# Kernel tuning notes

Measured on AMD Instinct MI355X. Metric: run time of the kernel, lower is better.

The kernel has to match this reference:

```python
import jax, jax.numpy as jnp
import numpy as np
from jax import lax

B, S, D, H, TMAX = 8, 512, 256, 4, 20
DH = D // H
LAMBDA = 1e-3
V_TH = 1.0


def setup_inputs() -> dict:
    key = jax.random.key(0)
    ks = jax.random.split(key, 10)
    sc = lambda n: 1.0 / np.sqrt(n)
    f32 = jnp.float32
    return {
        "x": jax.random.normal(ks[0], (B, S, D), f32),
        "Wq": (jax.random.normal(ks[1], (D, D), f32) * sc(D)),
        "Wk": (jax.random.normal(ks[2], (D, D), f32) * sc(D)),
        "Wv": (jax.random.normal(ks[3], (D, D), f32) * sc(D)),
        "Wo": (jax.random.normal(ks[4], (D, D), f32) * sc(D)),
        "bo": jnp.zeros((D,), f32),
        "Wg1": (jax.random.normal(ks[5], (D, 32), f32) * sc(D)),
        "bg1": jnp.zeros((32,), f32),
        "Wg2": (jax.random.normal(ks[6], (32, 1), f32) * sc(32)),
        "bg2": jnp.zeros((1,), f32),
        "alpha_q": jnp.asarray(np.exp(-1 / 5.0), f32),
        "beta_q": jnp.asarray(np.exp(-1 / 20.0), f32),
        "alpha_k": jnp.asarray(np.exp(-1 / 5.0), f32),
        "beta_k": jnp.asarray(np.exp(-1 / 20.0), f32),
        "alpha_v": jnp.asarray(np.exp(-1 / 5.0), f32),
        "beta_v": jnp.asarray(np.exp(-1 / 20.0), f32),
    }


def _lif_spikes(x, alpha, beta, Ti):
    """LIF recurrence with CONSTANT input x per step, sequential only over T.
    x: [B,S,D], Ti: [B,S] int. Returns spikes [B,S,TMAX,D], zeroed for t >= Ti
    (equivalent to the original per-(b,s) loop that only runs Ti steps,
    since the recurrence is causal)."""
    zeros = jnp.zeros_like(x)
    tmask = jnp.arange(TMAX)

    def step(carry, t):
        v, i = carry
        i = alpha * i + x
        v = beta * v + i
        spk = (v >= V_TH).astype(x.dtype)
        v = v * (1.0 - spk)  # v_reset = 0
        spk_out = spk * (t < Ti).astype(x.dtype)[..., None]
        return (v, i), spk_out

    _, spks = lax.scan(step, (zeros, zeros), tmask)
    return jnp.moveaxis(spks, 0, 2)  # [B,S,T,D]


def reference(x, Wq, Wk, Wv, Wo, bo, Wg1, bg1, Wg2, bg2,
              alpha_q, beta_q, alpha_k, beta_k, alpha_v, beta_v):
    q = x @ Wq
    k = x @ Wk
    v = x @ Wv
    # adaptive window gate -> Ti in [1, TMAX]
    gate = jax.nn.sigmoid(jax.nn.relu(x @ Wg1 + bg1) @ Wg2 + bg2)[..., 0]  # [B,S]
    Ti = jnp.clip(jnp.ceil(gate * TMAX), 1, TMAX).astype(jnp.int32)
    q_spk = _lif_spikes(q, alpha_q, beta_q, Ti)  # [B,S,T,D]
    k_spk = _lif_spikes(k, alpha_k, beta_k, Ti)
    v_spk = _lif_spikes(v, alpha_v, beta_v, Ti)
    qh = q_spk.reshape(B, S, TMAX, H, DH)
    kh = k_spk.reshape(B, S, TMAX, H, DH)
    vh = v_spk.reshape(B, S, TMAX, H, DH)
    scale = DH ** -0.5
    Sraw = jnp.einsum('bithd,bjthd->bhij', qh, kh) * scale  # [B,H,S,S]
    W = jax.nn.softmax(Sraw, axis=-1)
    v_mean = vh.mean(axis=2)  # [B,S,H,DH] (mean over full T, zeros beyond Ti)
    out = jnp.einsum('bhij,bjhd->bihd', W, v_mean).reshape(B, S, D)
    out = out @ Wo + bo
    reg = LAMBDA * Ti.astype(jnp.float32).mean()
    return out, reg, Ti, W
```

## Files before the change

### kernel.cpp

```cpp
#include <hip/hip_runtime.h>
#include <hip/hip_bf16.h>

typedef unsigned long long u64;
typedef unsigned short u16;
typedef __attribute__((ext_vector_type(8))) short short8;
typedef __attribute__((ext_vector_type(4))) float float4_t;

#define BB 8
#define SS 512
#define DD 256
#define HH 4
#define TT 20
#define BS (BB*SS)

#define REG_OFF (BS*DD)
#define TI_OFF  (REG_OFF+1)
#define W_OFF   (TI_OFF+BS)

static __device__ __forceinline__ u16 f2bf(float f) {
    __hip_bfloat16 h = __float2bfloat16(f);
    return *reinterpret_cast<u16*>(&h);
}

__global__ __launch_bounds__(256) void k_proj_lif(
    const float* __restrict__ x, const float* __restrict__ Wq,
    const float* __restrict__ Wk, const float* __restrict__ Wv,
    const float* __restrict__ Wg1, const float* __restrict__ bg1,
    const float* __restrict__ Wg2, const float* __restrict__ bg2,
    const float* __restrict__ aq, const float* __restrict__ bq_,
    const float* __restrict__ ak, const float* __restrict__ bk_,
    const float* __restrict__ av, const float* __restrict__ bv_,
    u64* __restrict__ qpack, u64* __restrict__ kpack,
    u16* __restrict__ vmb, float* __restrict__ ti_out)
{
    __shared__ float xl[8][DD];
    __shared__ int til[8];
    const int tid  = threadIdx.x;
    const int proj = blockIdx.y;
    const int tok0 = blockIdx.x * 8;

    #pragma unroll
    for (int m = 0; m < 8; ++m) xl[m][tid] = x[(size_t)(tok0+m)*DD + tid];
    __syncthreads();

    {
        int tok = tid >> 5, c = tid & 31;
        float acc = bg1[c];
        for (int r = 0; r < DD; ++r) acc += xl[tok][r] * Wg1[r*32 + c];
        float hrelu = acc > 0.f ? acc : 0.f;
        float term  = hrelu * Wg2[c];
        #pragma unroll
        for (int msk = 16; msk >= 1; msk >>= 1) term += __shfl_xor(term, msk, 64);
        if (c == 0) {
            float g  = term + bg2[0];
            float sg = 1.f / (1.f + expf(-g));
            int ti = (int)ceilf(sg * (float)TT);
            ti = ti < 1 ? 1 : (ti > TT ? TT : ti);
            til[tok] = ti;
            if (proj == 0) ti_out[tok0 + tok] = (float)ti;
        }
    }
    __syncthreads();

    const float* W    = proj == 0 ? Wq  : (proj == 1 ? Wk  : Wv);
    const float alpha = proj == 0 ? *aq : (proj == 1 ? *ak : *av);
    const float beta  = proj == 0 ? *bq_: (proj == 1 ? *bk_: *bv_);

    float acc[8] = {0,0,0,0,0,0,0,0};
    for (int r = 0; r < DD; ++r) {
        float w = W[r*DD + tid];
        #pragma unroll
        for (int i = 0; i < 8; ++i) acc[i] += xl[i][r] * w;
    }

    const int lane = tid & 63;
    const int h    = tid >> 6;
    u64* pack = (proj == 0) ? qpack : kpack;

    if (proj < 2) {
        for (int i = 0; i < 8; ++i) {
            int ti = til[i];
            float vv = 0.f, cur = 0.f;
            u64 myw = 0ull;
            #pragma unroll
            for (int t = 0; t < TT; ++t) {
                cur = alpha*cur + acc[i];
                vv  = beta*vv + cur;
                bool s = (vv >= 1.f);
                u64 bal = __ballot(s);
                if (s) vv = 0.f;
                if (lane == t && t < ti) myw = bal;
            }
            if (lane < TT) pack[((size_t)(tok0+i)*HH + h)*TT + lane] = myw;
        }
    } else {
        for (int i = 0; i < 8; ++i) {
            int ti = til[i];
            float vv = 0.f, cur = 0.f;
            float cnt = 0.f;
            #pragma unroll
            for (int t = 0; t < TT; ++t) {
                cur = alpha*cur + acc[i];
                vv  = beta*vv + cur;
                bool s = (vv >= 1.f);
                if (s) { vv = 0.f; if (t < ti) cnt += 1.f; }
            }
            vmb[(size_t)(tok0+i)*DD + tid] = f2bf(cnt * 0.05f);
        }
    }
}

__global__ __launch_bounds__(256) void k_reg(const float* __restrict__ ti, float* __restrict__ reg)
{
    __shared__ float ps[4];
    int tid = threadIdx.x;
    float s = 0.f;
    for (int m = 0; m < 16; ++m) s += ti[m*256 + tid];
    for (int msk = 32; msk >= 1; msk >>= 1) s += __shfl_xor(s, msk, 64);
    if ((tid & 63) == 0) ps[tid >> 6] = s;
    __syncthreads();
    if (tid == 0) reg[0] = 1e-3f * (ps[0]+ps[1]+ps[2]+ps[3]) / 4096.f;
}

__global__ __launch_bounds__(256) void k_attn(
    const u64* __restrict__ qpack, const u64* __restrict__ kpack,
    const u16* __restrict__ vmb,
    float* __restrict__ Wout, float* __restrict__ attn)
{
    __shared__ u64 ql[16][TT];
    __shared__ __align__(16) u16 CP[16*SS];
    const int tid  = threadIdx.x;
    const int tile = blockIdx.x & 31;
    const int h    = (blockIdx.x >> 5) & 3;
    const int b    = blockIdx.x >> 7;
    const int i0   = tile * 16;
    const int lane = tid & 63, wv = tid >> 6;

    for (int idx = tid; idx < 16*TT; idx += 256) {
        int i = idx / TT, t = idx - i*TT;
        ql[i][t] = qpack[((size_t)(b*SS + i0 + i)*HH + h)*TT + t];
    }

    u64 kr0[TT], kr1[TT];
    {
        const u64* kp0 = &kpack[((size_t)(b*SS + tid      )*HH + h)*TT];
        const u64* kp1 = &kpack[((size_t)(b*SS + tid + 256)*HH + h)*TT];
        #pragma unroll
        for (int t = 0; t < TT; ++t) { kr0[t] = kp0[t]; kr1[t] = kp1[t]; }
    }
    __syncthreads();

    for (int i = 0; i < 16; ++i) {
        int c0 = 0, c1 = 0;
        #pragma unroll
        for (int t = 0; t < TT; ++t) {
            u64 q = ql[i][t];
            c0 += __popcll(q & kr0[t]);
            c1 += __popcll(q & kr1[t]);
        }
        CP[i*SS + tid]       = (u16)c0;
        CP[i*SS + tid + 256] = (u16)c1;
    }
    __syncthreads();

    for (int rr = 0; rr < 4; ++rr) {
        const int i = wv*4 + rr;
        float sv[8];
        float m = -1e30f;
        #pragma unroll
        for (int k2 = 0; k2 < 8; ++k2) {
            sv[k2] = (float)CP[i*SS + lane + 64*k2] * 0.125f;
            m = fmaxf(m, sv[k2]);
        }
        #pragma unroll
        for (int msk = 32; msk >= 1; msk >>= 1) m = fmaxf(m, __shfl_xor(m, msk, 64));
        float sum = 0.f;
        #pragma unroll
        for (int k2 = 0; k2 < 8; ++k2) { sv[k2] = expf(sv[k2] - m); sum += sv[k2]; }
        #pragma unroll
        for (int msk = 32; msk >= 1; msk >>= 1) sum += __shfl_xor(sum, msk, 64);
        float inv = 1.f / sum;
        size_t wbase = ((size_t)((b*HH + h)*SS) + i0 + i) * SS;
        #pragma unroll
        for (int k2 = 0; k2 < 8; ++k2) {
            int j = lane + 64*k2;
            float wval = sv[k2] * inv;
            Wout[wbase + j] = wval;
            CP[(i*SS + j) ^ ((i & 7) << 3)] = f2bf(wval);
        }
    }
    __syncthreads();

    const int n0 = wv * 16;
    const int mr = lane & 15;
    const int g  = lane >> 4;
    float4_t acc = {0.f, 0.f, 0.f, 0.f};
    const u16* vb_base = vmb + (size_t)b*SS*DD + h*64 + n0 + mr;
    for (int ks = 0; ks < 16; ++ks) {
        int k = ks*32 + g*8;
        int aidx = (mr*SS + k) ^ ((mr & 7) << 3);
        short8 a = *reinterpret_cast<const short8*>(&CP[aidx]);
        union { u16 u[8]; short8 v; } bu;
        const u16* vb = vb_base + (size_t)k*DD;
        #pragma unroll
        for (int j = 0; j < 8; ++j) bu.u[j] = vb[(size_t)j*DD];
        acc = __builtin_amdgcn_mfma_f32_16x16x32_bf16(a, bu.v, acc, 0, 0, 0);
    }
    #pragma unroll
    for (int r = 0; r < 4; ++r) {
        int row = g*4 + r;
        attn[(size_t)(b*SS + i0 + row)*DD + h*64 + n0 + mr] = acc[r];
    }
}

__global__ __launch_bounds__(256) void k_outproj(
    const float* __restrict__ attn, const float* __restrict__ Wo,
    const float* __restrict__ bo, float* __restrict__ out)
{
    __shared__ float al[4][DD];
    const int tid  = threadIdx.x;
    const int tok0 = blockIdx.x * 4;
    #pragma unroll
    for (int m = 0; m < 4; ++m) al[m][tid] = attn[(size_t)(tok0+m)*DD + tid];
    __syncthreads();
    float acc[4] = {0,0,0,0};
    for (int r = 0; r < DD; ++r) {
        float w = Wo[r*DD + tid];
        #pragma unroll
        for (int i = 0; i < 4; ++i) acc[i] += al[i][r] * w;
    }
    float bb = bo[tid];
    #pragma unroll
    for (int i = 0; i < 4; ++i) out[(size_t)(tok0+i)*DD + tid] = acc[i] + bb;
}

extern "C" void kernel_launch(void* const* d_in, const int* in_sizes, int n_in,
                              void* d_out, int out_size, void* d_ws, size_t ws_size,
                              hipStream_t stream)
{
    (void)in_sizes; (void)n_in; (void)out_size; (void)ws_size;
    const float* x   = (const float*)d_in[0];
    const float* Wq  = (const float*)d_in[1];
    const float* Wk  = (const float*)d_in[2];
    const float* Wv  = (const float*)d_in[3];
    const float* Wo  = (const float*)d_in[4];
    const float* bo  = (const float*)d_in[5];
    const float* Wg1 = (const float*)d_in[6];
    const float* bg1 = (const float*)d_in[7];
    const float* Wg2 = (const float*)d_in[8];
    const float* bg2 = (const float*)d_in[9];
    const float* aq  = (const float*)d_in[10];
    const float* bq  = (const float*)d_in[11];
    const float* ak  = (const float*)d_in[12];
    const float* bk  = (const float*)d_in[13];
    const float* av  = (const float*)d_in[14];
    const float* bv  = (const float*)d_in[15];
    float* out = (float*)d_out;

    u64* qp = (u64*)d_ws;
    u64* kp = qp + (size_t)BS*HH*TT;
    u16* vmb = (u16*)(kp + (size_t)BS*HH*TT);
    float* attnbuf = (float*)(vmb + (size_t)BS*DD);

    dim3 gproj(512, 3);
    k_proj_lif<<<gproj, 256, 0, stream>>>(x, Wq, Wk, Wv, Wg1, bg1, Wg2, bg2,
        aq, bq, ak, bk, av, bv, qp, kp, vmb, out + TI_OFF);
    k_reg<<<1, 256, 0, stream>>>(out + TI_OFF, out + REG_OFF);
    k_attn<<<1024, 256, 0, stream>>>(qp, kp, vmb, out + W_OFF, attnbuf);
    k_outproj<<<1024, 256, 0, stream>>>(attnbuf, Wo, bo, out);
}
```

Measured before the change: 118.3 us.

## Split gate into separate kernel and transpose LDS tiles for vectorized projection loads

Moves the gate MLP out of the projection kernel into its own kernel, so it is computed once per token instead of once for each of the three projections; the projection kernel now reads Ti from global memory. The projection and output-projection kernels store the token tile transposed in shared memory, so each weight row pairs with two float4 LDS reads covering eight tokens. The output projection also processes eight tokens per block with half as many blocks, which doubles reuse of each Wo load. The cost is an extra kernel launch and a dependency between the gate and projection kernels.

```diff
diff --git a/kernel.cpp b/kernel.cpp
--- a/kernel.cpp
+++ b/kernel.cpp
@@ -22,44 +22,55 @@
     return *reinterpret_cast<u16*>(&h);
 }
 
+__global__ __launch_bounds__(256) void k_gate(
+    const float* __restrict__ x,
+    const float* __restrict__ Wg1, const float* __restrict__ bg1,
+    const float* __restrict__ Wg2, const float* __restrict__ bg2,
+    float* __restrict__ ti_out)
+{
+    __shared__ float xl[8][DD];
+    const int tid  = threadIdx.x;
+    const int tok0 = blockIdx.x * 8;
+    #pragma unroll
+    for (int m = 0; m < 8; ++m) xl[m][tid] = x[(size_t)(tok0+m)*DD + tid];
+    __syncthreads();
+
+    const int tok = tid >> 5, c = tid & 31;
+    float acc = bg1[c];
+    #pragma unroll 4
+    for (int r = 0; r < DD; ++r) acc += xl[tok][r] * Wg1[r*32 + c];
+    float hrelu = acc > 0.f ? acc : 0.f;
+    float term  = hrelu * Wg2[c];
+    #pragma unroll
+    for (int msk = 16; msk >= 1; msk >>= 1) term += __shfl_xor(term, msk, 64);
+    if (c == 0) {
+        float g  = term + bg2[0];
+        float sg = 1.f / (1.f + expf(-g));
+        int ti = (int)ceilf(sg * (float)TT);
+        ti = ti < 1 ? 1 : (ti > TT ? TT : ti);
+        ti_out[tok0 + tok] = (float)ti;
+    }
+}
+
 __global__ __launch_bounds__(256) void k_proj_lif(
     const float* __restrict__ x, const float* __restrict__ Wq,
     const float* __restrict__ Wk, const float* __restrict__ Wv,
-    const float* __restrict__ Wg1, const float* __restrict__ bg1,
-    const float* __restrict__ Wg2, const float* __restrict__ bg2,
     const float* __restrict__ aq, const float* __restrict__ bq_,
     const float* __restrict__ ak, const float* __restrict__ bk_,
     const float* __restrict__ av, const float* __restrict__ bv_,
+    const float* __restrict__ ti_in,
     u64* __restrict__ qpack, u64* __restrict__ kpack,
-    u16* __restrict__ vmb, float* __restrict__ ti_out)
-{
-    __shared__ float xl[8][DD];
+    u16* __restrict__ vmb)
+{
+    __shared__ float xl[DD][8];
     __shared__ int til[8];
     const int tid  = threadIdx.x;
     const int proj = blockIdx.y;
     const int tok0 = blockIdx.x * 8;
 
     #pragma unroll
-    for (int m = 0; m < 8; ++m) xl[m][tid] = x[(size_t)(tok0+m)*DD + tid];
-    __syncthreads();
-
-    {
-        int tok = tid >> 5, c = tid & 31;
-        float acc = bg1[c];
-        for (int r = 0; r < DD; ++r) acc += xl[tok][r] * Wg1[r*32 + c];
-        float hrelu = acc > 0.f ? acc : 0.f;
-        float term  = hrelu * Wg2[c];
-        #pragma unroll
-        for (int msk = 16; msk >= 1; msk >>= 1) term += __shfl_xor(term, msk, 64);
-        if (c == 0) {
-            float g  = term + bg2[0];
-            float sg = 1.f / (1.f + expf(-g));
-            int ti = (int)ceilf(sg * (float)TT);
-            ti = ti < 1 ? 1 : (ti > TT ? TT : ti);
-            til[tok] = ti;
-            if (proj == 0) ti_out[tok0 + tok] = (float)ti;
-        }
-    }
+    for (int m = 0; m < 8; ++m) xl[tid][m] = x[(size_t)(tok0+m)*DD + tid];
+    if (tid < 8) til[tid] = (int)ti_in[tok0 + tid];
     __syncthreads();
 
     const float* W    = proj == 0 ? Wq  : (proj == 1 ? Wk  : Wv);
@@ -67,10 +78,13 @@
     const float beta  = proj == 0 ? *bq_: (proj == 1 ? *bk_: *bv_);
 
     float acc[8] = {0,0,0,0,0,0,0,0};
+    #pragma unroll 4
     for (int r = 0; r < DD; ++r) {
         float w = W[r*DD + tid];
-        #pragma unroll
-        for (int i = 0; i < 8; ++i) acc[i] += xl[i][r] * w;
+        float4_t x0 = *reinterpret_cast<const float4_t*>(&xl[r][0]);
+        float4_t x1 = *reinterpret_cast<const float4_t*>(&xl[r][4]);
+        acc[0] += x0.x*w; acc[1] += x0.y*w; acc[2] += x0.z*w; acc[3] += x0.w*w;
+        acc[4] += x1.x*w; acc[5] += x1.y*w; acc[6] += x1.z*w; acc[7] += x1.w*w;
     }
 
     const int lane = tid & 63;
@@ -217,21 +231,24 @@
     const float* __restrict__ attn, const float* __restrict__ Wo,
     const float* __restrict__ bo, float* __restrict__ out)
 {
-    __shared__ float al[4][DD];
-    const int tid  = threadIdx.x;
-    const int tok0 = blockIdx.x * 4;
-    #pragma unroll
-    for (int m = 0; m < 4; ++m) al[m][tid] = attn[(size_t)(tok0+m)*DD + tid];
-    __syncthreads();
-    float acc[4] = {0,0,0,0};
+    __shared__ float al[DD][8];
+    const int tid  = threadIdx.x;
+    const int tok0 = blockIdx.x * 8;
+    #pragma unroll
+    for (int m = 0; m < 8; ++m) al[tid][m] = attn[(size_t)(tok0+m)*DD + tid];
+    __syncthreads();
+    float acc[8] = {0,0,0,0,0,0,0,0};
+    #pragma unroll 4
     for (int r = 0; r < DD; ++r) {
         float w = Wo[r*DD + tid];
-        #pragma unroll
-        for (int i = 0; i < 4; ++i) acc[i] += al[i][r] * w;
+        float4_t a0 = *reinterpret_cast<const float4_t*>(&al[r][0]);
+        float4_t a1 = *reinterpret_cast<const float4_t*>(&al[r][4]);
+        acc[0] += a0.x*w; acc[1] += a0.y*w; acc[2] += a0.z*w; acc[3] += a0.w*w;
+        acc[4] += a1.x*w; acc[5] += a1.y*w; acc[6] += a1.z*w; acc[7] += a1.w*w;
     }
     float bb = bo[tid];
     #pragma unroll
-    for (int i = 0; i < 4; ++i) out[(size_t)(tok0+i)*DD + tid] = acc[i] + bb;
+    for (int i = 0; i < 8; ++i) out[(size_t)(tok0+i)*DD + tid] = acc[i] + bb;
 }
 
 extern "C" void kernel_launch(void* const* d_in, const int* in_sizes, int n_in,
@@ -262,10 +279,11 @@
     u16* vmb = (u16*)(kp + (size_t)BS*HH*TT);
     float* attnbuf = (float*)(vmb + (size_t)BS*DD);
 
+    k_gate<<<512, 256, 0, stream>>>(x, Wg1, bg1, Wg2, bg2, out + TI_OFF);
+    k_reg<<<1, 256, 0, stream>>>(out + TI_OFF, out + REG_OFF);
     dim3 gproj(512, 3);
-    k_proj_lif<<<gproj, 256, 0, stream>>>(x, Wq, Wk, Wv, Wg1, bg1, Wg2, bg2,
-        aq, bq, ak, bk, av, bv, qp, kp, vmb, out + TI_OFF);
-    k_reg<<<1, 256, 0, stream>>>(out + TI_OFF, out + REG_OFF);
+    k_proj_lif<<<gproj, 256, 0, stream>>>(x, Wq, Wk, Wv,
+        aq, bq, ak, bk, av, bv, out + TI_OFF, qp, kp, vmb);
     k_attn<<<1024, 256, 0, stream>>>(qp, kp, vmb, out + W_OFF, attnbuf);
-    k_outproj<<<1024, 256, 0, stream>>>(attnbuf, Wo, bo, out);
-}
+    k_outproj<<<512, 256, 0, stream>>>(attnbuf, Wo, bo, out);
+}
```

After: 127.1 us. 7.5% more time.

## Split gate kernel, retile projections with float4 split-K, transpose V means for attention

Applied to the files above, without the earlier changes.

Moves the gate MLP into its own kernel so it is no longer recomputed by all three projection blocks. The Q/K/V and output projections now process 16 tokens per 512-thread block using float4 weight loads and a two-way split-K reduction through shared memory. V spike means are stored transposed so the attention MFMA B-fragment becomes one 16-byte load instead of eight strided loads. The reg reduction is folded into the output projection kernel. The cost is an extra launch plus added shared-memory traffic and barriers for the split-K reduction.

```diff
diff --git a/kernel.cpp b/kernel.cpp
--- a/kernel.cpp
+++ b/kernel.cpp
@@ -22,109 +22,159 @@
     return *reinterpret_cast<u16*>(&h);
 }
 
-__global__ __launch_bounds__(256) void k_proj_lif(
+__global__ __launch_bounds__(256) void k_gate(
+    const float* __restrict__ x,
+    const float* __restrict__ Wg1, const float* __restrict__ bg1,
+    const float* __restrict__ Wg2, const float* __restrict__ bg2,
+    float* __restrict__ ti_out)
+{
+    __shared__ float wgl[DD*32];
+    __shared__ float xl[16][DD];
+    const int tid  = threadIdx.x;
+    const int tok0 = blockIdx.x * 16;
+
+    #pragma unroll
+    for (int i = 0; i < 8; ++i) {
+        int j = i*256 + tid;
+        *reinterpret_cast<float4_t*>(&wgl[j*4]) =
+            *reinterpret_cast<const float4_t*>(&Wg1[j*4]);
+    }
+    #pragma unroll
+    for (int m = 0; m < 16; ++m) xl[m][tid] = x[(size_t)(tok0+m)*DD + tid];
+    __syncthreads();
+
+    const int tok = tid >> 4;
+    const int cq  = tid & 15;
+    const int c   = cq * 2;
+    float a0 = 0.f, a1 = 0.f;
+    #pragma unroll 8
+    for (int r = 0; r < DD; ++r) {
+        float xv = xl[tok][r];
+        a0 += xv * wgl[r*32 + c];
+        a1 += xv * wgl[r*32 + c + 1];
+    }
+    a0 += bg1[c]; a1 += bg1[c+1];
+    a0 = a0 > 0.f ? a0 : 0.f;
+    a1 = a1 > 0.f ? a1 : 0.f;
+    float term = a0 * Wg2[c] + a1 * Wg2[c+1];
+    #pragma unroll
+    for (int msk = 8; msk >= 1; msk >>= 1) term += __shfl_xor(term, msk, 64);
+    if (cq == 0) {
+        float g  = term + bg2[0];
+        float sg = 1.f / (1.f + expf(-g));
+        int ti = (int)ceilf(sg * (float)TT);
+        ti = ti < 1 ? 1 : (ti > TT ? TT : ti);
+        ti_out[tok0 + tok] = (float)ti;
+    }
+}
+
+__global__ __launch_bounds__(512) void k_proj_lif(
     const float* __restrict__ x, const float* __restrict__ Wq,
     const float* __restrict__ Wk, const float* __restrict__ Wv,
-    const float* __restrict__ Wg1, const float* __restrict__ bg1,
-    const float* __restrict__ Wg2, const float* __restrict__ bg2,
     const float* __restrict__ aq, const float* __restrict__ bq_,
     const float* __restrict__ ak, const float* __restrict__ bk_,
     const float* __restrict__ av, const float* __restrict__ bv_,
+    const float* __restrict__ ti_in,
     u64* __restrict__ qpack, u64* __restrict__ kpack,
-    u16* __restrict__ vmb, float* __restrict__ ti_out)
-{
-    __shared__ float xl[8][DD];
-    __shared__ int til[8];
+    u16* __restrict__ vmbT)
+{
+    __shared__ __align__(16) union {
+        float xt[DD][16];
+        float red[2][16][DD];
+    } sm;
+    __shared__ int til[16];
     const int tid  = threadIdx.x;
     const int proj = blockIdx.y;
-    const int tok0 = blockIdx.x * 8;
-
-    #pragma unroll
-    for (int m = 0; m < 8; ++m) xl[m][tid] = x[(size_t)(tok0+m)*DD + tid];
-    __syncthreads();
+    const int tok0 = blockIdx.x * 16;
 
     {
-        int tok = tid >> 5, c = tid & 31;
-        float acc = bg1[c];
-        for (int r = 0; r < DD; ++r) acc += xl[tok][r] * Wg1[r*32 + c];
-        float hrelu = acc > 0.f ? acc : 0.f;
-        float term  = hrelu * Wg2[c];
-        #pragma unroll
-        for (int msk = 16; msk >= 1; msk >>= 1) term += __shfl_xor(term, msk, 64);
-        if (c == 0) {
-            float g  = term + bg2[0];
-            float sg = 1.f / (1.f + expf(-g));
-            int ti = (int)ceilf(sg * (float)TT);
-            ti = ti < 1 ? 1 : (ti > TT ? TT : ti);
-            til[tok] = ti;
-            if (proj == 0) ti_out[tok0 + tok] = (float)ti;
-        }
-    }
+        const int r = tid & 255, mh = tid >> 8;
+        #pragma unroll
+        for (int i = 0; i < 8; ++i) {
+            int m = mh*8 + i;
+            sm.xt[r][m] = x[(size_t)(tok0+m)*DD + r];
+        }
+    }
+    if (tid < 16) til[tid] = (int)ti_in[tok0 + tid];
     __syncthreads();
 
     const float* W    = proj == 0 ? Wq  : (proj == 1 ? Wk  : Wv);
     const float alpha = proj == 0 ? *aq : (proj == 1 ? *ak : *av);
     const float beta  = proj == 0 ? *bq_: (proj == 1 ? *bk_: *bv_);
 
-    float acc[8] = {0,0,0,0,0,0,0,0};
-    for (int r = 0; r < DD; ++r) {
-        float w = W[r*DD + tid];
-        #pragma unroll
-        for (int i = 0; i < 8; ++i) acc[i] += xl[i][r] * w;
+    const int w  = tid >> 6, l = tid & 63;
+    const int kh = w >> 2;
+    const int tg = w & 3;
+
+    float4_t a[4];
+    #pragma unroll
+    for (int i = 0; i < 4; ++i) a[i] = (float4_t){0.f, 0.f, 0.f, 0.f};
+
+    const float* Wp = W + (size_t)(kh*128)*DD + l*4;
+    #pragma unroll 4
+    for (int r0 = 0; r0 < 128; ++r0) {
+        float4_t wf = *reinterpret_cast<const float4_t*>(Wp + (size_t)r0*DD);
+        float4_t xv = *reinterpret_cast<const float4_t*>(&sm.xt[kh*128 + r0][tg*4]);
+        a[0] += wf*xv.x; a[1] += wf*xv.y; a[2] += wf*xv.z; a[3] += wf*xv.w;
+    }
+    __syncthreads();
+    #pragma unroll
+    for (int i = 0; i < 4; ++i)
+        *reinterpret_cast<float4_t*>(&sm.red[kh][tg*4 + i][l*4]) = a[i];
+    __syncthreads();
+
+    const int col = tid & 255, th = tid >> 8;
+    float val[8];
+    #pragma unroll
+    for (int i = 0; i < 8; ++i) {
+        int m = th*8 + i;
+        val[i] = sm.red[0][m][col] + sm.red[1][m][col];
     }
 
     const int lane = tid & 63;
-    const int h    = tid >> 6;
-    u64* pack = (proj == 0) ? qpack : kpack;
-
+    const int h    = (tid >> 6) & 3;
     if (proj < 2) {
+        u64* pack = (proj == 0) ? qpack : kpack;
         for (int i = 0; i < 8; ++i) {
-            int ti = til[i];
+            const int m  = th*8 + i;
+            const int ti = til[m];
             float vv = 0.f, cur = 0.f;
             u64 myw = 0ull;
             #pragma unroll
             for (int t = 0; t < TT; ++t) {
-                cur = alpha*cur + acc[i];
+                cur = alpha*cur + val[i];
                 vv  = beta*vv + cur;
                 bool s = (vv >= 1.f);
                 u64 bal = __ballot(s);
                 if (s) vv = 0.f;
                 if (lane == t && t < ti) myw = bal;
             }
-            if (lane < TT) pack[((size_t)(tok0+i)*HH + h)*TT + lane] = myw;
+            if (lane < TT)
+                pack[((size_t)(tok0+m)*HH + h)*TT + lane] = myw;
         }
     } else {
+        u16 tmp[8];
         for (int i = 0; i < 8; ++i) {
-            int ti = til[i];
-            float vv = 0.f, cur = 0.f;
-            float cnt = 0.f;
+            const int m  = th*8 + i;
+            const int ti = til[m];
+            float vv = 0.f, cur = 0.f, cnt = 0.f;
             #pragma unroll
             for (int t = 0; t < TT; ++t) {
-                cur = alpha*cur + acc[i];
+                cur = alpha*cur + val[i];
                 vv  = beta*vv + cur;
                 bool s = (vv >= 1.f);
                 if (s) { vv = 0.f; if (t < ti) cnt += 1.f; }
             }
-            vmb[(size_t)(tok0+i)*DD + tid] = f2bf(cnt * 0.05f);
-        }
-    }
-}
-
-__global__ __launch_bounds__(256) void k_reg(const float* __restrict__ ti, float* __restrict__ reg)
-{
-    __shared__ float ps[4];
-    int tid = threadIdx.x;
-    float s = 0.f;
-    for (int m = 0; m < 16; ++m) s += ti[m*256 + tid];
-    for (int msk = 32; msk >= 1; msk >>= 1) s += __shfl_xor(s, msk, 64);
-    if ((tid & 63) == 0) ps[tid >> 6] = s;
-    __syncthreads();
-    if (tid == 0) reg[0] = 1e-3f * (ps[0]+ps[1]+ps[2]+ps[3]) / 4096.f;
+            tmp[i] = f2bf(cnt * 0.05f);
+        }
+        *reinterpret_cast<short8*>(&vmbT[(size_t)col*BS + tok0 + th*8]) =
+            *reinterpret_cast<short8*>(tmp);
+    }
 }
 
 __global__ __launch_bounds__(256) void k_attn(
     const u64* __restrict__ qpack, const u64* __restrict__ kpack,
-    const u16* __restrict__ vmb,
+    const u16* __restrict__ vmbT,
     float* __restrict__ Wout, float* __restrict__ attn)
 {
     __shared__ u64 ql[16][TT];
@@ -195,16 +245,13 @@
     const int mr = lane & 15;
     const int g  = lane >> 4;
     float4_t acc = {0.f, 0.f, 0.f, 0.f};
-    const u16* vb_base = vmb + (size_t)b*SS*DD + h*64 + n0 + mr;
+    const u16* vbT = vmbT + (size_t)(h*64 + n0 + mr)*BS + b*SS;
     for (int ks = 0; ks < 16; ++ks) {
         int k = ks*32 + g*8;
         int aidx = (mr*SS + k) ^ ((mr & 7) << 3);
-        short8 a = *reinterpret_cast<const short8*>(&CP[aidx]);
-        union { u16 u[8]; short8 v; } bu;
-        const u16* vb = vb_base + (size_t)k*DD;
-        #pragma unroll
-        for (int j = 0; j < 8; ++j) bu.u[j] = vb[(size_t)j*DD];
-        acc = __builtin_amdgcn_mfma_f32_16x16x32_bf16(a, bu.v, acc, 0, 0, 0);
+        short8 afrag = *reinterpret_cast<const short8*>(&CP[aidx]);
+        short8 bfrag = *reinterpret_cast<const short8*>(vbT + k);
+        acc = __builtin_amdgcn_mfma_f32_16x16x32_bf16(afrag, bfrag, acc, 0, 0, 0);
     }
     #pragma unroll
     for (int r = 0; r < 4; ++r) {
@@ -213,25 +260,71 @@
     }
 }
 
-__global__ __launch_bounds__(256) void k_outproj(
+__global__ __launch_bounds__(512) void k_outproj(
     const float* __restrict__ attn, const float* __restrict__ Wo,
-    const float* __restrict__ bo, float* __restrict__ out)
-{
-    __shared__ float al[4][DD];
+    const float* __restrict__ bo, const float* __restrict__ ti,
+    float* __restrict__ out)
+{
+    __shared__ __align__(16) union {
+        float xt[DD][16];
+        float red[2][16][DD];
+    } sm;
+    __shared__ float ps[8];
     const int tid  = threadIdx.x;
-    const int tok0 = blockIdx.x * 4;
-    #pragma unroll
-    for (int m = 0; m < 4; ++m) al[m][tid] = attn[(size_t)(tok0+m)*DD + tid];
-    __syncthreads();
-    float acc[4] = {0,0,0,0};
-    for (int r = 0; r < DD; ++r) {
-        float w = Wo[r*DD + tid];
-        #pragma unroll
-        for (int i = 0; i < 4; ++i) acc[i] += al[i][r] * w;
-    }
-    float bb = bo[tid];
-    #pragma unroll
-    for (int i = 0; i < 4; ++i) out[(size_t)(tok0+i)*DD + tid] = acc[i] + bb;
+    const int tok0 = blockIdx.x * 16;
+
+    {
+        const int r = tid & 255, mh = tid >> 8;
+        #pragma unroll
+        for (int i = 0; i < 8; ++i) {
+            int m = mh*8 + i;
+            sm.xt[r][m] = attn[(size_t)(tok0+m)*DD + r];
+        }
+    }
+    __syncthreads();
+
+    const int w  = tid >> 6, l = tid & 63;
+    const int kh = w >> 2, tg = w & 3;
+
+    float4_t a[4];
+    #pragma unroll
+    for (int i = 0; i < 4; ++i) a[i] = (float4_t){0.f, 0.f, 0.f, 0.f};
+    const float* Wp = Wo + (size_t)(kh*128)*DD + l*4;
+    #pragma unroll 4
+    for (int r0 = 0; r0 < 128; ++r0) {
+        float4_t wf = *reinterpret_cast<const float4_t*>(Wp + (size_t)r0*DD);
+        float4_t xv = *reinterpret_cast<const float4_t*>(&sm.xt[kh*128 + r0][tg*4]);
+        a[0] += wf*xv.x; a[1] += wf*xv.y; a[2] += wf*xv.z; a[3] += wf*xv.w;
+    }
+    __syncthreads();
+    #pragma unroll
+    for (int i = 0; i < 4; ++i)
+        *reinterpret_cast<float4_t*>(&sm.red[kh][tg*4 + i][l*4]) = a[i];
+    __syncthreads();
+
+    const int col = tid & 255, th = tid >> 8;
+    float bb = bo[col];
+    #pragma unroll
+    for (int i = 0; i < 8; ++i) {
+        int m = th*8 + i;
+        float v = sm.red[0][m][col] + sm.red[1][m][col];
+        out[(size_t)(tok0+m)*DD + col] = v + bb;
+    }
+
+    if (blockIdx.x == 0) {
+        float s = 0.f;
+        if (tid < 256) for (int m = 0; m < 16; ++m) s += ti[m*256 + tid];
+        #pragma unroll
+        for (int msk = 32; msk >= 1; msk >>= 1) s += __shfl_xor(s, msk, 64);
+        if ((tid & 63) == 0) ps[tid >> 6] = s;
+        __syncthreads();
+        if (tid == 0) {
+            float t = 0.f;
+            #pragma unroll
+            for (int i = 0; i < 8; ++i) t += ps[i];
+            out[REG_OFF] = 1e-3f * t / 4096.f;
+        }
+    }
 }
 
 extern "C" void kernel_launch(void* const* d_in, const int* in_sizes, int n_in,
@@ -259,13 +352,13 @@
 
     u64* qp = (u64*)d_ws;
     u64* kp = qp + (size_t)BS*HH*TT;
-    u16* vmb = (u16*)(kp + (size_t)BS*HH*TT);
-    float* attnbuf = (float*)(vmb + (size_t)BS*DD);
-
-    dim3 gproj(512, 3);
-    k_proj_lif<<<gproj, 256, 0, stream>>>(x, Wq, Wk, Wv, Wg1, bg1, Wg2, bg2,
-        aq, bq, ak, bk, av, bv, qp, kp, vmb, out + TI_OFF);
-    k_reg<<<1, 256, 0, stream>>>(out + TI_OFF, out + REG_OFF);
-    k_attn<<<1024, 256, 0, stream>>>(qp, kp, vmb, out + W_OFF, attnbuf);
-    k_outproj<<<1024, 256, 0, stream>>>(attnbuf, Wo, bo, out);
-}
+    u16* vmbT = (u16*)(kp + (size_t)BS*HH*TT);
+    float* attnbuf = (float*)(vmbT + (size_t)BS*DD);
+
+    k_gate<<<256, 256, 0, stream>>>(x, Wg1, bg1, Wg2, bg2, out + TI_OFF);
+    dim3 gproj(256, 3);
+    k_proj_lif<<<gproj, 512, 0, stream>>>(x, Wq, Wk, Wv,
+        aq, bq, ak, bk, av, bv, out + TI_OFF, qp, kp, vmbT);
+    k_attn<<<1024, 256, 0, stream>>>(qp, kp, vmbT, out + W_OFF, attnbuf);
+    k_outproj<<<256, 512, 0, stream>>>(attnbuf, Wo, bo, out + TI_OFF, out);
+}
```

Measured after the change: 105.1 us. 11.1% less time.
